# Kernel optimization log

Hardware: AMD Instinct MI355X
Metric: run time of the kernel (lower is better)

Reference implementation:

```python
import jax, jax.numpy as jnp
import numpy as np

BATCH, SEQ, D_MODEL, D_STATE = 16, 1024, 512, 32
DT_MIN, DT_MAX, DT_FLOOR = 1e-3, 1e-1, 1e-4


def _init_ssm(key):
    k1, k2, k3, k4 = jax.random.split(key, 4)
    scale = 1.0 / np.sqrt(D_STATE)
    z = jax.random.normal(k1, (D_MODEL, D_STATE)) * scale
    A_log = -jnp.exp(z)  # A = exp(A_log) in (0,1)
    B = jax.random.normal(k2, (D_MODEL, D_STATE)) * scale
    C = jax.random.normal(k3, (D_MODEL, D_STATE)) * scale
    log_dt = jax.random.uniform(k4, (D_MODEL,)) * (np.log(DT_MAX) - np.log(DT_MIN)) + np.log(DT_MIN)
    log_dt = jnp.maximum(log_dt, np.log(DT_FLOOR))
    return A_log, B, C, log_dt


def setup_inputs() -> dict:
    key = jax.random.key(0)
    kx, khr, kbr = jax.random.split(key, 3)
    x = jax.random.normal(kx, (BATCH, SEQ, D_MODEL), dtype=jnp.float32)
    A_log_hr, B_hr, C_hr, log_dt_hr = _init_ssm(khr)
    A_log_br, B_br, C_br, log_dt_br = _init_ssm(kbr)
    return dict(
        x=x,
        A_log_hr=A_log_hr, B_hr=B_hr, C_hr=C_hr, log_dt_hr=log_dt_hr,
        A_log_br=A_log_br, B_br=B_br, C_br=C_br, log_dt_br=log_dt_br,
        weight_hr=jnp.ones((D_MODEL,), jnp.float32),
        weight_br=jnp.ones((D_MODEL,), jnp.float32),
    )


def _ssm(x, A_log, B, C, log_dt):
    # delta=None path: dt = exp(log_dt) * dt_scale(=1), time-invariant -> dA, dB are [d, n]
    dt = jnp.exp(log_dt)                 # [d]
    A = jnp.exp(A_log)                   # [d, n]
    dA = jnp.exp(dt[:, None] * A)        # [d, n]  (matches torch: exp(dt*exp(A_log)))
    dB = dt[:, None] * B                 # [d, n]
    b = x.shape[0]
    h0 = jnp.zeros((b, A.shape[0], A.shape[1]), x.dtype)  # [b, d, n]

    def step(h, xt):  # xt: [b, d]
        h = dA * h + dB * xt[:, :, None]
        y = jnp.einsum('bdn,dn->bd', h, C)
        return h, y

    _, ys = jax.lax.scan(step, h0, jnp.swapaxes(x, 0, 1))  # ys: [L, b, d]
    return jnp.swapaxes(ys, 0, 1)        # [b, L, d]


def reference(x, A_log_hr, B_hr, C_hr, log_dt_hr,
              A_log_br, B_br, C_br, log_dt_br,
              weight_hr, weight_br):
    x_hr = _ssm(x, A_log_hr, B_hr, C_hr, log_dt_hr) * weight_hr  # [b, L, d]
    x_br = _ssm(x, A_log_br, B_br, C_br, log_dt_br) * weight_br
    return (x_hr, x_br, x_hr + x_br)  # hr_enhanced, br_enhanced, combined
```

## Files before the change

### kernel.cpp

```cpp
#include <hip/hip_runtime.h>

#define BATCH 16
#define SEQ   1024
#define DM    512
#define NST   32
#define PF    8

#define PIN(v) asm volatile("" : "+v"(v))

__global__ __launch_bounds__(256) void ssm_setup(
    const float* __restrict__ Alog_hr, const float* __restrict__ B_hr,
    const float* __restrict__ C_hr,    const float* __restrict__ ldt_hr,
    const float* __restrict__ Alog_br, const float* __restrict__ B_br,
    const float* __restrict__ C_br,    const float* __restrict__ ldt_br,
    const float* __restrict__ w_hr,    const float* __restrict__ w_br,
    float* __restrict__ dA_tbl, float* __restrict__ Cw_tbl)
{
    int idx = blockIdx.x * blockDim.x + threadIdx.x;
    int d   = idx & (DM - 1);
    int n   = (idx >> 9) & (NST - 1);
    int ssm = idx >> 14;

    const float* Alog = ssm ? Alog_br : Alog_hr;
    const float* Bm   = ssm ? B_br    : B_hr;
    const float* Cm   = ssm ? C_br    : C_hr;
    const float* ldt  = ssm ? ldt_br  : ldt_hr;
    const float* w    = ssm ? w_br    : w_hr;

    float dt = expf(ldt[d]);
    float a  = expf(Alog[d * NST + n]);
    dA_tbl[idx] = expf(dt * a);
    Cw_tbl[idx] = Cm[d * NST + n] * Bm[d * NST + n] * dt * w[d];
}

__global__ __launch_bounds__(256) void ssm_pass1(
    const float* __restrict__ x,
    const float* __restrict__ dA_tbl,
    float* __restrict__ ws_state, int nc, int cl)
{
    int tid  = threadIdx.x;
    int dlo  = tid & 127;
    int nh   = tid >> 7;
    int bid  = blockIdx.x;
    int dblk = bid & 3;
    int r    = bid >> 2;
    int c    = r % nc;  r /= nc;
    int b    = r & (BATCH - 1);
    int ssm  = r >> 4;
    int d    = dblk * 128 + dlo;
    int n0   = nh * 16;

    const float* tb = dA_tbl + ((size_t)ssm * NST + n0) * DM + d;
    float dA[16], g[16];
#pragma unroll
    for (int i = 0; i < 16; ++i) {
        dA[i] = tb[(size_t)i * DM];
        g[i]  = 0.f;
    }
#pragma unroll
    for (int i = 0; i < 16; ++i) PIN(dA[i]);

    const float* xp = x + ((size_t)b * SEQ + (size_t)c * cl) * DM + d;

    float xf[PF];
#pragma unroll
    for (int k = 0; k < PF; ++k) xf[k] = xp[(size_t)k * DM];
    const float* xq = xp + (size_t)PF * DM;

    int ntb = cl / PF;
    for (int t8 = 0; t8 < ntb - 1; ++t8) {
#pragma unroll
        for (int j = 0; j < PF; ++j) {
            float xv = xf[j];
            xf[j] = xq[(size_t)j * DM];
#pragma unroll
            for (int i = 0; i < 16; ++i) g[i] = fmaf(dA[i], g[i], xv);
        }
        xq += (size_t)PF * DM;
    }
#pragma unroll
    for (int j = 0; j < PF; ++j) {
        float xv = xf[j];
#pragma unroll
        for (int i = 0; i < 16; ++i) g[i] = fmaf(dA[i], g[i], xv);
    }

    float* sp = ws_state + ((((size_t)ssm * BATCH + b) * nc + c) * NST + n0) * DM + d;
#pragma unroll
    for (int i = 0; i < 16; ++i) sp[(size_t)i * DM] = g[i];
}

__global__ __launch_bounds__(256) void ssm_pass2(
    const float* __restrict__ Alog_hr, const float* __restrict__ ldt_hr,
    const float* __restrict__ Alog_br, const float* __restrict__ ldt_br,
    float* __restrict__ ws_state, int nc, int cl)
{
    int idx = blockIdx.x * blockDim.x + threadIdx.x;
    int d   = idx & (DM - 1);
    int n   = (idx >> 9) & (NST - 1);
    int b   = (idx >> 14) & 15;
    int ssm = idx >> 18;

    const float* Alog = ssm ? Alog_br : Alog_hr;
    const float* ldt  = ssm ? ldt_br  : ldt_hr;

    float dt = expf(ldt[d]);
    float A  = expf(Alog[d * NST + n]);
    float p  = expf((float)cl * dt * A);

    float* sp = ws_state + ((((size_t)ssm * BATCH + b) * nc) * NST + n) * DM + d;
    size_t cstride = (size_t)NST * DM;

    float H = 0.f;
    for (int c = 0; c < nc; ++c) {
        float s = *sp;
        *sp = H;
        H = fmaf(p, H, s);
        sp += cstride;
    }
}

__global__ __launch_bounds__(128, 2) void ssm_pass3(
    const float* __restrict__ x,
    const float* __restrict__ dA_tbl, const float* __restrict__ Cw_tbl,
    const float* __restrict__ ws_state,
    float* __restrict__ out_hr, float* __restrict__ out_br, float* __restrict__ out_cb,
    int nc, int cl)
{
    int tid  = threadIdx.x;
    int lane = tid & 63;
    int wid  = tid >> 6;
    int ssm  = lane >> 5;
    int dlo  = lane & 31;
    int bid  = blockIdx.x;
    int dblk = bid & 7;
    int r    = bid >> 3;
    int c    = r % nc;
    int b    = r / nc;
    int d    = dblk * 64 + wid * 32 + dlo;

    const float* dat = dA_tbl + (size_t)ssm * NST * DM + d;
    const float* cwt = Cw_tbl + (size_t)ssm * NST * DM + d;
    float dA[NST], Cw[NST];
#pragma unroll
    for (int n = 0; n < NST; ++n) {
        dA[n] = dat[(size_t)n * DM];
        Cw[n] = cwt[(size_t)n * DM];
    }
#pragma unroll
    for (int n = 0; n < NST; ++n) { PIN(dA[n]); PIN(Cw[n]); }

    float g[NST];
    if (c == 0) {
#pragma unroll
        for (int n = 0; n < NST; ++n) g[n] = 0.f;
    } else {
        const float* sp = ws_state + ((((size_t)ssm * BATCH + b) * nc + c) * NST) * DM + d;
#pragma unroll
        for (int n = 0; n < NST; ++n) g[n] = sp[(size_t)n * DM];
    }

    size_t off = ((size_t)b * SEQ + (size_t)c * cl) * DM + d;
    const float* xp = x + off;
    float* oh = out_hr + off;
    float* ob = out_br + off;
    float* oc = out_cb + off;

    float xf[PF];
#pragma unroll
    for (int k = 0; k < PF; ++k) xf[k] = xp[(size_t)k * DM];
    const float* xq = xp + (size_t)PF * DM;

#define BODY(xv)                                                        \
    {                                                                   \
        float y0 = 0.f, y1 = 0.f, y2 = 0.f, y3 = 0.f;                   \
        _Pragma("unroll")                                               \
        for (int n = 0; n < NST; n += 4) {                              \
            g[n]     = fmaf(dA[n],     g[n],     xv);                   \
            g[n + 1] = fmaf(dA[n + 1], g[n + 1], xv);                   \
            g[n + 2] = fmaf(dA[n + 2], g[n + 2], xv);                   \
            g[n + 3] = fmaf(dA[n + 3], g[n + 3], xv);                   \
            y0 = fmaf(Cw[n],     g[n],     y0);                         \
            y1 = fmaf(Cw[n + 1], g[n + 1], y1);                         \
            y2 = fmaf(Cw[n + 2], g[n + 2], y2);                         \
            y3 = fmaf(Cw[n + 3], g[n + 3], y3);                         \
        }                                                               \
        float y  = (y0 + y1) + (y2 + y3);                               \
        float yo = __shfl_xor(y, 32, 64);                               \
        if (ssm == 0) { *oh = y; *oc = y + yo; }                        \
        else          { *ob = y; }                                      \
        oh += DM;  ob += DM;  oc += DM;                                 \
    }

    int ntb = cl / PF;
    for (int t8 = 0; t8 < ntb - 1; ++t8) {
#pragma unroll
        for (int j = 0; j < PF; ++j) {
            float xv = xf[j];
            xf[j] = xq[(size_t)j * DM];
            BODY(xv);
        }
        xq += (size_t)PF * DM;
    }
#pragma unroll
    for (int j = 0; j < PF; ++j) {
        float xv = xf[j];
        BODY(xv);
    }
#undef BODY
}

extern "C" void kernel_launch(void* const* d_in, const int* in_sizes, int n_in,
                              void* d_out, int out_size, void* d_ws, size_t ws_size,
                              hipStream_t stream)
{
    (void)in_sizes; (void)n_in; (void)out_size;

    const float* x       = (const float*)d_in[0];
    const float* Alog_hr = (const float*)d_in[1];
    const float* B_hr    = (const float*)d_in[2];
    const float* C_hr    = (const float*)d_in[3];
    const float* ldt_hr  = (const float*)d_in[4];
    const float* Alog_br = (const float*)d_in[5];
    const float* B_br    = (const float*)d_in[6];
    const float* C_br    = (const float*)d_in[7];
    const float* ldt_br  = (const float*)d_in[8];
    const float* w_hr    = (const float*)d_in[9];
    const float* w_br    = (const float*)d_in[10];

    float* out    = (float*)d_out;
    const size_t one = (size_t)BATCH * SEQ * DM;
    float* out_hr = out;
    float* out_br = out + one;
    float* out_cb = out + 2 * one;

    float* dA_tbl = (float*)d_ws;
    float* Cw_tbl = dA_tbl + (size_t)2 * NST * DM;
    float* ws_st  = Cw_tbl + (size_t)2 * NST * DM;

    const size_t tbl_bytes = (size_t)4 * NST * DM * sizeof(float);
    int nc = 8;
    while (nc > 1 &&
           ws_size < tbl_bytes + (size_t)2 * BATCH * nc * NST * DM * sizeof(float))
        nc >>= 1;
    int cl = SEQ / nc;

    int total0 = 2 * NST * DM;
    ssm_setup<<<total0 / 256, 256, 0, stream>>>(Alog_hr, B_hr, C_hr, ldt_hr,
                                                Alog_br, B_br, C_br, ldt_br,
                                                w_hr, w_br, dA_tbl, Cw_tbl);

    if (nc > 1) {
        int nblk1 = 2 * BATCH * nc * 4;
        ssm_pass1<<<nblk1, 256, 0, stream>>>(x, dA_tbl, ws_st, nc, cl);
        int total2 = 2 * BATCH * NST * DM;
        ssm_pass2<<<total2 / 256, 256, 0, stream>>>(Alog_hr, ldt_hr, Alog_br, ldt_br,
                                                    ws_st, nc, cl);
    }

    int nblk3 = BATCH * nc * 8;
    ssm_pass3<<<nblk3, 128, 0, stream>>>(x, dA_tbl, Cw_tbl, ws_st,
                                         out_hr, out_br, out_cb, nc, cl);
}
```

Before: 76.70 us.

## Fuse setup and carry-propagation kernels into chunked scan passes

Removes the separate setup and inter-chunk carry kernels. Pass1 now computes dA on the fly and skips the last chunk. Pass3 derives its starting state by folding the preceding chunk end-states with the chunk decay power. This cuts two kernel launches and their serialization, but pass3 does redundant exp work and reads up to nc-1 state slabs per block, so later chunks take on more load imbalance.

```diff
diff --git a/kernel.cpp b/kernel.cpp
--- a/kernel.cpp
+++ b/kernel.cpp
@@ -8,35 +8,12 @@
 
 #define PIN(v) asm volatile("" : "+v"(v))
 
-__global__ __launch_bounds__(256) void ssm_setup(
-    const float* __restrict__ Alog_hr, const float* __restrict__ B_hr,
-    const float* __restrict__ C_hr,    const float* __restrict__ ldt_hr,
-    const float* __restrict__ Alog_br, const float* __restrict__ B_br,
-    const float* __restrict__ C_br,    const float* __restrict__ ldt_br,
-    const float* __restrict__ w_hr,    const float* __restrict__ w_br,
-    float* __restrict__ dA_tbl, float* __restrict__ Cw_tbl)
-{
-    int idx = blockIdx.x * blockDim.x + threadIdx.x;
-    int d   = idx & (DM - 1);
-    int n   = (idx >> 9) & (NST - 1);
-    int ssm = idx >> 14;
-
-    const float* Alog = ssm ? Alog_br : Alog_hr;
-    const float* Bm   = ssm ? B_br    : B_hr;
-    const float* Cm   = ssm ? C_br    : C_hr;
-    const float* ldt  = ssm ? ldt_br  : ldt_hr;
-    const float* w    = ssm ? w_br    : w_hr;
-
-    float dt = expf(ldt[d]);
-    float a  = expf(Alog[d * NST + n]);
-    dA_tbl[idx] = expf(dt * a);
-    Cw_tbl[idx] = Cm[d * NST + n] * Bm[d * NST + n] * dt * w[d];
-}
 
 __global__ __launch_bounds__(256) void ssm_pass1(
     const float* __restrict__ x,
-    const float* __restrict__ dA_tbl,
-    float* __restrict__ ws_state, int nc, int cl)
+    const float* __restrict__ Alog_hr, const float* __restrict__ ldt_hr,
+    const float* __restrict__ Alog_br, const float* __restrict__ ldt_br,
+    float* __restrict__ E, int nc, int cl)
 {
     int tid  = threadIdx.x;
     int dlo  = tid & 127;
@@ -44,17 +21,21 @@
     int bid  = blockIdx.x;
     int dblk = bid & 3;
     int r    = bid >> 2;
-    int c    = r % nc;  r /= nc;
+    int ncm1 = nc - 1;
+    int c    = r % ncm1;  r /= ncm1;
     int b    = r & (BATCH - 1);
     int ssm  = r >> 4;
     int d    = dblk * 128 + dlo;
     int n0   = nh * 16;
 
-    const float* tb = dA_tbl + ((size_t)ssm * NST + n0) * DM + d;
+    const float* Alog = ssm ? Alog_br : Alog_hr;
+    const float* ldt  = ssm ? ldt_br  : ldt_hr;
+
+    float dt = expf(ldt[d]);
     float dA[16], g[16];
 #pragma unroll
     for (int i = 0; i < 16; ++i) {
-        dA[i] = tb[(size_t)i * DM];
+        dA[i] = expf(dt * expf(Alog[d * NST + n0 + i]));
         g[i]  = 0.f;
     }
 #pragma unroll
@@ -85,45 +66,19 @@
         for (int i = 0; i < 16; ++i) g[i] = fmaf(dA[i], g[i], xv);
     }
 
-    float* sp = ws_state + ((((size_t)ssm * BATCH + b) * nc + c) * NST + n0) * DM + d;
+    float* sp = E + ((((size_t)ssm * BATCH + b) * nc + c) * NST + n0) * DM + d;
 #pragma unroll
     for (int i = 0; i < 16; ++i) sp[(size_t)i * DM] = g[i];
 }
 
-__global__ __launch_bounds__(256) void ssm_pass2(
-    const float* __restrict__ Alog_hr, const float* __restrict__ ldt_hr,
-    const float* __restrict__ Alog_br, const float* __restrict__ ldt_br,
-    float* __restrict__ ws_state, int nc, int cl)
-{
-    int idx = blockIdx.x * blockDim.x + threadIdx.x;
-    int d   = idx & (DM - 1);
-    int n   = (idx >> 9) & (NST - 1);
-    int b   = (idx >> 14) & 15;
-    int ssm = idx >> 18;
-
-    const float* Alog = ssm ? Alog_br : Alog_hr;
-    const float* ldt  = ssm ? ldt_br  : ldt_hr;
-
-    float dt = expf(ldt[d]);
-    float A  = expf(Alog[d * NST + n]);
-    float p  = expf((float)cl * dt * A);
-
-    float* sp = ws_state + ((((size_t)ssm * BATCH + b) * nc) * NST + n) * DM + d;
-    size_t cstride = (size_t)NST * DM;
-
-    float H = 0.f;
-    for (int c = 0; c < nc; ++c) {
-        float s = *sp;
-        *sp = H;
-        H = fmaf(p, H, s);
-        sp += cstride;
-    }
-}
-
 __global__ __launch_bounds__(128, 2) void ssm_pass3(
     const float* __restrict__ x,
-    const float* __restrict__ dA_tbl, const float* __restrict__ Cw_tbl,
-    const float* __restrict__ ws_state,
+    const float* __restrict__ Alog_hr, const float* __restrict__ B_hr,
+    const float* __restrict__ C_hr,    const float* __restrict__ ldt_hr,
+    const float* __restrict__ Alog_br, const float* __restrict__ B_br,
+    const float* __restrict__ C_br,    const float* __restrict__ ldt_br,
+    const float* __restrict__ w_hr,    const float* __restrict__ w_br,
+    const float* __restrict__ E,
     float* __restrict__ out_hr, float* __restrict__ out_br, float* __restrict__ out_cb,
     int nc, int cl)
 {
@@ -139,26 +94,43 @@
     int b    = r / nc;
     int d    = dblk * 64 + wid * 32 + dlo;
 
-    const float* dat = dA_tbl + (size_t)ssm * NST * DM + d;
-    const float* cwt = Cw_tbl + (size_t)ssm * NST * DM + d;
+    const float* Alog = ssm ? Alog_br : Alog_hr;
+    const float* Bm   = ssm ? B_br    : B_hr;
+    const float* Cm   = ssm ? C_br    : C_hr;
+    const float* ldt  = ssm ? ldt_br  : ldt_hr;
+    const float* w    = ssm ? w_br    : w_hr;
+
+    float dt = expf(ldt[d]);
+    float wd = w[d];
+
+    float A[NST], g[NST];
+#pragma unroll
+    for (int n = 0; n < NST; ++n) {
+        A[n] = expf(Alog[d * NST + n]);
+        g[n] = 0.f;
+    }
+    {
+        float p[NST];
+#pragma unroll
+        for (int n = 0; n < NST; ++n) p[n] = expf((float)cl * dt * A[n]);
+        const size_t slab = (size_t)NST * DM;
+        const float* ep = E + (((size_t)ssm * BATCH + b) * nc) * slab + d;
+        for (int cc = 0; cc < c; ++cc) {
+#pragma unroll
+            for (int n = 0; n < NST; ++n)
+                g[n] = fmaf(p[n], g[n], ep[(size_t)n * DM]);
+            ep += slab;
+        }
+    }
+
     float dA[NST], Cw[NST];
 #pragma unroll
     for (int n = 0; n < NST; ++n) {
-        dA[n] = dat[(size_t)n * DM];
-        Cw[n] = cwt[(size_t)n * DM];
+        dA[n] = expf(dt * A[n]);
+        Cw[n] = Cm[d * NST + n] * Bm[d * NST + n] * dt * wd;
     }
 #pragma unroll
     for (int n = 0; n < NST; ++n) { PIN(dA[n]); PIN(Cw[n]); }
-
-    float g[NST];
-    if (c == 0) {
-#pragma unroll
-        for (int n = 0; n < NST; ++n) g[n] = 0.f;
-    } else {
-        const float* sp = ws_state + ((((size_t)ssm * BATCH + b) * nc + c) * NST) * DM + d;
-#pragma unroll
-        for (int n = 0; n < NST; ++n) g[n] = sp[(size_t)n * DM];
-    }
 
     size_t off = ((size_t)b * SEQ + (size_t)c * cl) * DM + d;
     const float* xp = x + off;
@@ -234,31 +206,24 @@
     float* out_br = out + one;
     float* out_cb = out + 2 * one;
 
-    float* dA_tbl = (float*)d_ws;
-    float* Cw_tbl = dA_tbl + (size_t)2 * NST * DM;
-    float* ws_st  = Cw_tbl + (size_t)2 * NST * DM;
-
-    const size_t tbl_bytes = (size_t)4 * NST * DM * sizeof(float);
+    float* E = (float*)d_ws;
+
     int nc = 8;
     while (nc > 1 &&
-           ws_size < tbl_bytes + (size_t)2 * BATCH * nc * NST * DM * sizeof(float))
+           ws_size < (size_t)2 * BATCH * nc * NST * DM * sizeof(float))
         nc >>= 1;
     int cl = SEQ / nc;
 
-    int total0 = 2 * NST * DM;
-    ssm_setup<<<total0 / 256, 256, 0, stream>>>(Alog_hr, B_hr, C_hr, ldt_hr,
-                                                Alog_br, B_br, C_br, ldt_br,
-                                                w_hr, w_br, dA_tbl, Cw_tbl);
-
     if (nc > 1) {
-        int nblk1 = 2 * BATCH * nc * 4;
-        ssm_pass1<<<nblk1, 256, 0, stream>>>(x, dA_tbl, ws_st, nc, cl);
-        int total2 = 2 * BATCH * NST * DM;
-        ssm_pass2<<<total2 / 256, 256, 0, stream>>>(Alog_hr, ldt_hr, Alog_br, ldt_br,
-                                                    ws_st, nc, cl);
+        int nblk1 = 2 * BATCH * (nc - 1) * 4;
+        ssm_pass1<<<nblk1, 256, 0, stream>>>(x, Alog_hr, ldt_hr, Alog_br, ldt_br,
+                                             E, nc, cl);
     }
 
     int nblk3 = BATCH * nc * 8;
-    ssm_pass3<<<nblk3, 128, 0, stream>>>(x, dA_tbl, Cw_tbl, ws_st,
+    ssm_pass3<<<nblk3, 128, 0, stream>>>(x,
+                                         Alog_hr, B_hr, C_hr, ldt_hr,
+                                         Alog_br, B_br, C_br, ldt_br,
+                                         w_hr, w_br, E,
                                          out_hr, out_br, out_cb, nc, cl);
 }
```

After: 74.76 us. 2.5% less time.
